# Optimization experiments

Measured on AMD Instinct MI355X. Metric: run time of the kernel, lower is better.

## Reference

```python
import jax, jax.numpy as jnp
import numpy as np
import math

DIM = 1024
H = 16
DH = DIM // H
B = 2
L = 1024


def setup_inputs() -> dict:
    key = jax.random.key(0)
    ks = jax.random.split(key, 8)
    s = 1.0 / math.sqrt(DIM)
    return {
        "Q": jax.random.normal(ks[0], (B, L, DIM), jnp.float32),
        "K": jax.random.normal(ks[1], (B, L, DIM), jnp.float32),
        "mask_Q": jax.random.bernoulli(ks[2], 0.1, (B, L)),
        "mask_K": jax.random.bernoulli(ks[3], 0.1, (B, L)),
        "Wq": jax.random.normal(ks[4], (DIM, DIM), jnp.float32) * s,
        "Wk": jax.random.normal(ks[5], (DIM, DIM), jnp.float32) * s,
        "Wv": jax.random.normal(ks[6], (DIM, DIM), jnp.float32) * s,
        "Wo": jax.random.normal(ks[7], (DIM, DIM), jnp.float32) * s,
    }


def reference(Q, K, mask_Q, mask_K, Wq, Wk, Wv, Wo):
    # V defaults to K. Masked positions of inputs are zeroed first.
    Qz = jnp.where(mask_Q[:, :, None], 0.0, Q)
    Kz = jnp.where(mask_K[:, :, None], 0.0, K)
    Vz = Kz  # V = K, masked with mask_K

    # Projections (nn.Linear, no bias): y = x @ W.T
    Qp = jnp.einsum('bld,ed->ble', Qz, Wq)
    Kp = jnp.einsum('bld,ed->ble', Kz, Wk)
    Vp = jnp.einsum('bld,ed->ble', Vz, Wv)

    # split heads: [B, L, H, DH] -> per-head attention
    qh = Qp.reshape(B, L, H, DH)
    kh = Kp.reshape(B, L, H, DH)
    vh = Vp.reshape(B, L, H, DH)

    # NOTE: original scales by sqrt(dim) (full dim), not sqrt(dim_split)
    scores = jnp.einsum('bqhd,bkhd->bhqk', qh, kh) / math.sqrt(DIM)

    # outer-product validity mask: valid iff both q and k positions unmasked
    valid = (~mask_Q)[:, None, :, None] & (~mask_K)[:, None, None, :]  # [B,1,Lq,Lk]
    A = jnp.where(valid, scores, -1e38)
    A = jax.nn.softmax(A, axis=-1)
    A = jnp.where(valid, A, 0.0)

    O = jnp.einsum('bhqk,bkhd->bqhd', A, vh).reshape(B, L, DIM)
    # residual uses the PROJECTED Q (Q was reassigned to fc_q(Q) in torch)
    O = Qp + O
    # masked_forward(fc_o, ...): fc_o applied, masked query rows forced to 0
    ff = jax.nn.relu(jnp.where(mask_Q[:, :, None], 0.0, jnp.einsum('bld,ed->ble', O, Wo)))
    O = O + ff
    return O
```

## Files before the change

kernel.cpp:

```cpp
#include <hip/hip_runtime.h>
#include <hip/hip_bf16.h>


#define DEV __device__ __forceinline__

typedef __attribute__((ext_vector_type(8))) short bf16x8;
typedef __attribute__((ext_vector_type(4))) float f32x4;
typedef __hip_bfloat16 bf16;

DEV void glds16(const bf16* g, bf16* s) {
  __builtin_amdgcn_global_load_lds(
      (const __attribute__((address_space(1))) void*)g,
      (__attribute__((address_space(3))) void*)s, 16, 0, 0);
}

DEV unsigned short f2bu(float x) {
  __hip_bfloat16 b = __float2bfloat16(x);
  unsigned short u;
  __builtin_memcpy(&u, &b, 2);
  return u;
}

DEV float bu2f(unsigned short u) {
  unsigned int v = (unsigned int)u << 16;
  float f;
  __builtin_memcpy(&f, &v, 4);
  return f;
}

__global__ void normalize_masks(const unsigned char* mq_raw, const unsigned char* mk_raw,
                                unsigned char* outq, unsigned char* outk,
                                unsigned long long* qm64, unsigned long long* km64) {
  __shared__ int cnt;
  int t = threadIdx.x;
  if (t == 0) cnt = 0;
  __syncthreads();
  int c = 0;
  for (int i = t; i < 2048; i += 256) c += (mq_raw[i] != 0);
  atomicAdd(&cnt, c);
  __syncthreads();
  bool isByte = cnt > 128;
  for (int i = t; i < 2048; i += 256) {
    unsigned char q, k;
    if (isByte) {
      q = (mq_raw[i] != 0); k = (mk_raw[i] != 0);
    } else {
      q = (((const int*)mq_raw)[i] != 0); k = (((const int*)mk_raw)[i] != 0);
    }
    outq[i] = q; outk[i] = k;
  }
  __syncthreads();
  if (t < 64) {
    const unsigned char* src = (t < 32) ? outk : outq;
    int idx = t & 31;
    unsigned long long m = 0;
    for (int j = 0; j < 64; ++j)
      m |= (unsigned long long)(src[idx * 64 + j] != 0) << j;
    if (t < 32) km64[idx] = m; else qm64[idx] = m;
  }
}

__global__ __launch_bounds__(256) void cast_all(
    const float* __restrict__ Q, const float* __restrict__ K,
    const unsigned char* __restrict__ mq, const unsigned char* __restrict__ mk,
    const float* __restrict__ W0, const float* __restrict__ W1,
    const float* __restrict__ W2, const float* __restrict__ W3,
    bf16* __restrict__ Qz, bf16* __restrict__ Kz,
    bf16* __restrict__ o0, bf16* __restrict__ o1,
    bf16* __restrict__ o2, bf16* __restrict__ o3) {
  const int z = blockIdx.z;
  if (z < 2) {
    const float* X = z ? K : Q;
    const unsigned char* m = z ? mk : mq;
    bf16* out = z ? Kz : Qz;
    int i = (blockIdx.x * 256 + threadIdx.x) * 8;
    float4 v0 = *(const float4*)&X[i];
    float4 v1 = *(const float4*)&X[i + 4];
    if (m[i >> 10]) {
      v0 = make_float4(0.f, 0.f, 0.f, 0.f);
      v1 = make_float4(0.f, 0.f, 0.f, 0.f);
    }
    *(ushort4*)&out[i] = make_ushort4(f2bu(v0.x), f2bu(v0.y), f2bu(v0.z), f2bu(v0.w));
    *(ushort4*)&out[i + 4] = make_ushort4(f2bu(v1.x), f2bu(v1.y), f2bu(v1.z), f2bu(v1.w));
  } else {
    const float* X; bf16* out;
    switch (z) {
      case 2: X = W0; out = o0; break;
      case 3: X = W1; out = o1; break;
      case 4: X = W2; out = o2; break;
      default: X = W3; out = o3; break;
    }
    int i = (blockIdx.x * 256 + threadIdx.x) * 4;
    float4 v = *(const float4*)&X[i];
    *(ushort4*)&out[i] = make_ushort4(f2bu(v.x), f2bu(v.y), f2bu(v.z), f2bu(v.w));
  }
}

template <int MI, int NI, typename EPI>
DEV void gemm_core(const bf16* __restrict__ A, const bf16* __restrict__ W,
                   int K, int brow, int bcol, EPI&& epi) {
  __shared__ bf16 As[2 * MI * 512];
  __shared__ bf16 Bs[2 * NI * 2048];
  const int t = threadIdx.x, l = t & 63, w = t >> 6;
  const int rs = l >> 2;
  const int kcol = (l & 3) * 8;

  f32x4 acc[MI][NI];
#pragma unroll
  for (int i = 0; i < MI; i++)
#pragma unroll
    for (int j = 0; j < NI; j++) acc[i][j] = (f32x4){0.f, 0.f, 0.f, 0.f};

  auto stage = [&](int k0, int b_) {
#pragma unroll
    for (int i = 0; i < MI; ++i)
      if ((i & 3) == w)
        glds16(A + (size_t)(brow + i * 16 + rs) * K + k0 + kcol,
               &As[b_ * MI * 512 + i * 512]);
#pragma unroll
    for (int c = 0; c < NI; ++c)
      glds16(W + (size_t)(bcol + (w * NI + c) * 16 + rs) * K + k0 + kcol,
             &Bs[b_ * NI * 2048 + (w * NI + c) * 512]);
  };

  const int aoff0 = (l & 15) * 32 + (l >> 4) * 8;
  const int boff0 = (w * NI * 16 + (l & 15)) * 32 + (l >> 4) * 8;

  stage(0, 0);
  int buf = 0;
  for (int k0 = 0; k0 < K; k0 += 32) {
    __syncthreads();
    if (k0 + 32 < K) stage(k0 + 32, buf ^ 1);
    bf16x8 a[MI], b[NI];
#pragma unroll
    for (int mi = 0; mi < MI; ++mi)
      a[mi] = *(const bf16x8*)&As[buf * MI * 512 + aoff0 + mi * 512];
#pragma unroll
    for (int ni = 0; ni < NI; ++ni)
      b[ni] = *(const bf16x8*)&Bs[buf * NI * 2048 + boff0 + ni * 512];
#pragma unroll
    for (int mi = 0; mi < MI; ++mi)
#pragma unroll
      for (int ni = 0; ni < NI; ++ni)
        acc[mi][ni] = __builtin_amdgcn_mfma_f32_16x16x32_bf16(a[mi], b[ni], acc[mi][ni], 0, 0, 0);
    buf ^= 1;
  }

#pragma unroll
  for (int mi = 0; mi < MI; ++mi)
#pragma unroll
    for (int ni = 0; ni < NI; ++ni)
#pragma unroll
      for (int r = 0; r < 4; ++r) {
        int row = brow + mi * 16 + (l >> 4) * 4 + r;
        int col = bcol + (w * NI + ni) * 16 + (l & 15);
        epi(row, col, acc[mi][ni][r]);
      }
}

__global__ __launch_bounds__(256) void proj_gemm(
    const bf16* __restrict__ Qz, const bf16* __restrict__ Kz,
    const bf16* __restrict__ Wq, const bf16* __restrict__ Wk, const bf16* __restrict__ Wv,
    bf16* __restrict__ Qpb, bf16* __restrict__ Kpb, bf16* __restrict__ Vpb) {
  const int z = blockIdx.z;
  const int brow = blockIdx.x * 64, bcol = blockIdx.y * 128;
  const bf16* A = (z == 0) ? Qz : Kz;
  const bf16* W = (z == 0) ? Wq : ((z == 1) ? Wk : Wv);
  bf16* dst = (z == 0) ? Qpb : ((z == 1) ? Kpb : Vpb);
  const float scale = (z == 0) ? 0.045084220f : 1.0f;
  gemm_core<4, 2>(A, W, 1024, brow, bcol, [&](int row, int col, float v) {
    dst[((size_t)row << 10) + col] = __float2bfloat16(v * scale);
  });
}

__global__ __launch_bounds__(256) void final_gemm(
    const bf16* __restrict__ Ob, const bf16* __restrict__ Wo,
    float* __restrict__ out, const unsigned char* __restrict__ mq) {
  const int brow = blockIdx.x * 64, bcol = blockIdx.y * 64;
  gemm_core<4, 1>(Ob, Wo, 1024, brow, bcol, [&](int row, int col, float v) {
    size_t idx = ((size_t)row << 10) + col;
    float ff = mq[row] ? 0.f : fmaxf(v, 0.f);
    out[idx] = out[idx] + ff;
  });
}

__global__ __launch_bounds__(256) void attn_fused(
    const bf16* __restrict__ Qpb, const bf16* __restrict__ Kpb, const bf16* __restrict__ Vpb,
    const unsigned long long* __restrict__ qm64, const unsigned long long* __restrict__ km64,
    float* __restrict__ Of, bf16* __restrict__ Ob) {
  __shared__ bf16 Klds[2][64 * 64];
  __shared__ bf16 Vt[64 * 72];

  const int t = threadIdx.x, l = t & 63, w = t >> 6;
  const int q = l & 15, g = l >> 4;
  const int f = blockIdx.x;
  const int bh = (f & 7) + 8 * ((f >> 3) & 3);
  const int qt = f >> 5;
  const int b = bh >> 4, h = bh & 15;
  const size_t bbase = (size_t)b * 1024;

  const int qg = qt * 64 + w * 16 + q;
  const bf16* qptr = Qpb + (bbase + qg) * 1024 + h * 64 + g * 8;
  const bf16x8 qb0 = *(const bf16x8*)qptr;
  const bf16x8 qb1 = *(const bf16x8*)(qptr + 32);

  float psum = 0.f;
  f32x4 oacc[4];
#pragma unroll
  for (int mf = 0; mf < 4; ++mf) oacc[mf] = (f32x4){0.f, 0.f, 0.f, 0.f};

  const int krow_s = l >> 3;
  const int kcol_s = ((l & 7) ^ krow_s) * 8;
  const int vk0 = 2 * (t & 31);
  const int vdc = t >> 5;

  union { uint4 v; unsigned short s[8]; } u0, u1;

  auto stageK = [&](int kt_, int b_) {
#pragma unroll
    for (int c = 0; c < 2; ++c) {
      int cw = w * 2 + c;
      glds16(Kpb + (bbase + kt_ * 64 + cw * 8 + krow_s) * 1024 + h * 64 + kcol_s,
             &Klds[b_][cw * 512]);
    }
  };
  auto loadV = [&](int kt_) {
    const bf16* g0 = Vpb + (bbase + kt_ * 64 + vk0) * 1024 + h * 64 + vdc * 8;
    u0.v = *(const uint4*)g0;
    u1.v = *(const uint4*)(g0 + 1024);
  };

  stageK(0, 0);
  loadV(0);
  int buf = 0;

  for (int kt = 0; kt < 16; ++kt) {
    const unsigned long long km = km64[b * 16 + kt];
    const unsigned long long mloc = km >> (4 * g);

    __syncthreads();

#pragma unroll
    for (int j = 0; j < 8; ++j) {
      unsigned int pk = (unsigned int)u0.s[j] | ((unsigned int)u1.s[j] << 16);
      *(unsigned int*)((char*)Vt + (vdc * 8 + j) * 144 + vk0 * 2) = pk;
    }

    f32x4 S[4];
#pragma unroll
    for (int mf = 0; mf < 4; ++mf) {
#pragma unroll
      for (int r = 0; r < 4; ++r)
        S[mf][r] = ((mloc >> (mf * 16 + r)) & 1ull) ? -1e30f : 0.f;
      const int row = mf * 16 + q;
      const int rowb = row * 128;
      const bf16x8 ka0 = *(const bf16x8*)((const char*)&Klds[buf][0] + rowb + ((g ^ (row & 7)) * 16));
      const bf16x8 ka1 = *(const bf16x8*)((const char*)&Klds[buf][0] + rowb + (((g + 4) ^ (row & 7)) * 16));
      S[mf] = __builtin_amdgcn_mfma_f32_16x16x32_bf16(ka0, qb0, S[mf], 0, 0, 0);
      S[mf] = __builtin_amdgcn_mfma_f32_16x16x32_bf16(ka1, qb1, S[mf], 0, 0, 0);
    }

    unsigned int lo[4], hi[4];
#pragma unroll
    for (int mf = 0; mf < 4; ++mf) {
      float p0 = exp2f(S[mf][0]), p1 = exp2f(S[mf][1]);
      float p2 = exp2f(S[mf][2]), p3 = exp2f(S[mf][3]);
      psum += (p0 + p1) + (p2 + p3);
      lo[mf] = (unsigned int)f2bu(p0) | ((unsigned int)f2bu(p1) << 16);
      hi[mf] = (unsigned int)f2bu(p2) | ((unsigned int)f2bu(p3) << 16);
    }

    __syncthreads();

    if (kt < 15) {
      stageK(kt + 1, buf ^ 1);
      loadV(kt + 1);
    }

    const int srcA = ((2 * g) & 3) * 16 + q;
    const int srcB = srcA + 16;
    const bool sel = (g >> 1) & 1;
#pragma unroll
    for (int ks = 0; ks < 2; ++ks) {
      unsigned int a0 = __shfl(lo[2 * ks], srcA), a1 = __shfl(hi[2 * ks], srcA);
      unsigned int a2 = __shfl(lo[2 * ks], srcB), a3 = __shfl(hi[2 * ks], srcB);
      unsigned int b0 = __shfl(lo[2 * ks + 1], srcA), b1 = __shfl(hi[2 * ks + 1], srcA);
      unsigned int b2 = __shfl(lo[2 * ks + 1], srcB), b3 = __shfl(hi[2 * ks + 1], srcB);
      uint4 pw;
      pw.x = sel ? b0 : a0; pw.y = sel ? b1 : a1;
      pw.z = sel ? b2 : a2; pw.w = sel ? b3 : a3;
      const bf16x8 pa = __builtin_bit_cast(bf16x8, pw);
#pragma unroll
      for (int mf = 0; mf < 4; ++mf) {
        const bf16x8 va = *(const bf16x8*)((const char*)Vt + (mf * 16 + q) * 144 + ks * 64 + g * 16);
        oacc[mf] = __builtin_amdgcn_mfma_f32_16x16x32_bf16(va, pa, oacc[mf], 0, 0, 0);
      }
    }
    buf ^= 1;
  }

  psum += __shfl_xor(psum, 16);
  psum += __shfl_xor(psum, 32);

  const unsigned long long qm = qm64[b * 16 + qt];
  const bool qvalid = !((qm >> (w * 16 + q)) & 1ull);
  const float inv = (qvalid && psum > 0.f) ? 1.f / psum : 0.f;
  const float RQ = 22.180709777918f;
#pragma unroll
  for (int mf = 0; mf < 4; ++mf) {
    size_t idx = (bbase + qg) * 1024 + h * 64 + mf * 16 + g * 4;
    ushort4 q4 = *(const ushort4*)&Qpb[idx];
    float4 val;
    val.x = bu2f(q4.x) * RQ + oacc[mf][0] * inv;
    val.y = bu2f(q4.y) * RQ + oacc[mf][1] * inv;
    val.z = bu2f(q4.z) * RQ + oacc[mf][2] * inv;
    val.w = bu2f(q4.w) * RQ + oacc[mf][3] * inv;
    *(float4*)&Of[idx] = val;
    *(ushort4*)&Ob[idx] = make_ushort4(f2bu(val.x), f2bu(val.y), f2bu(val.z), f2bu(val.w));
  }
}

extern "C" void kernel_launch(void* const* d_in, const int* in_sizes, int n_in,
                              void* d_out, int out_size, void* d_ws, size_t ws_size,
                              hipStream_t stream) {
  const float* Q = (const float*)d_in[0];
  const float* K = (const float*)d_in[1];
  const unsigned char* mQraw = (const unsigned char*)d_in[2];
  const unsigned char* mKraw = (const unsigned char*)d_in[3];
  const float* Wq = (const float*)d_in[4];
  const float* Wk = (const float*)d_in[5];
  const float* Wv = (const float*)d_in[6];
  const float* Wo = (const float*)d_in[7];
  float* out = (float*)d_out;

  char* ws = (char*)d_ws;
  const size_t MB = 1024 * 1024;
  bf16* Qz = (bf16*)(ws + 0);
  bf16* Kz = (bf16*)(ws + 4 * MB);
  bf16* Wqb = (bf16*)(ws + 8 * MB);
  bf16* Wkb = (bf16*)(ws + 10 * MB);
  bf16* Wvb = (bf16*)(ws + 12 * MB);
  bf16* Wob = (bf16*)(ws + 14 * MB);
  bf16* Qpb = (bf16*)(ws + 16 * MB);
  bf16* Kpb = (bf16*)(ws + 20 * MB);
  bf16* Vpb = (bf16*)(ws + 24 * MB);
  bf16* Ob  = (bf16*)(ws + 28 * MB);
  unsigned char* mqn = (unsigned char*)(ws + 32 * MB);
  unsigned char* mkn = mqn + 2048;
  unsigned long long* km64 = (unsigned long long*)(ws + 32 * MB + 4096);
  unsigned long long* qm64 = km64 + 32;

  normalize_masks<<<1, 256, 0, stream>>>(mQraw, mKraw, mqn, mkn, qm64, km64);

  dim3 gc(1024, 1, 6);
  cast_all<<<gc, 256, 0, stream>>>(Q, K, mqn, mkn, Wq, Wk, Wv, Wo,
                                   Qz, Kz, Wqb, Wkb, Wvb, Wob);

  dim3 gp(32, 8, 3);
  proj_gemm<<<gp, 256, 0, stream>>>(Qz, Kz, Wqb, Wkb, Wvb, Qpb, Kpb, Vpb);

  attn_fused<<<512, 256, 0, stream>>>(Qpb, Kpb, Vpb, qm64, km64, out, Ob);

  dim3 gf(32, 16);
  final_gemm<<<gf, 256, 0, stream>>>(Ob, Wob, out, mqn);
}
```

Before: 96.54 us.

## Fuse fp32-to-bf16 casting and input masking into projection and output GEMM loads

Removes the separate cast_all kernel. The projection and output GEMMs now read fp32 activations and weights directly, apply the masks and convert to bf16 in registers before writing to shared memory. This saves one launch and the bf16 intermediate write and read. In exchange, the GEMMs load twice the bytes per tile through registers instead of the async global-to-LDS path. Weights are reconverted by every block that reads them, so conversion work repeats across blocks.

```diff
diff --git a/kernel.cpp b/kernel.cpp
--- a/kernel.cpp
+++ b/kernel.cpp
@@ -26,6 +26,15 @@
   float f;
   __builtin_memcpy(&f, &v, 4);
   return f;
+}
+
+DEV bf16x8 cvt8(float4 a, float4 b) {
+  bf16x8 r;
+  r[0] = (short)f2bu(a.x); r[1] = (short)f2bu(a.y);
+  r[2] = (short)f2bu(a.z); r[3] = (short)f2bu(a.w);
+  r[4] = (short)f2bu(b.x); r[5] = (short)f2bu(b.y);
+  r[6] = (short)f2bu(b.z); r[7] = (short)f2bu(b.w);
+  return r;
 }
 
 __global__ void normalize_masks(const unsigned char* mq_raw, const unsigned char* mk_raw,
@@ -60,128 +69,150 @@
   }
 }
 
-__global__ __launch_bounds__(256) void cast_all(
-    const float* __restrict__ Q, const float* __restrict__ K,
-    const unsigned char* __restrict__ mq, const unsigned char* __restrict__ mk,
-    const float* __restrict__ W0, const float* __restrict__ W1,
-    const float* __restrict__ W2, const float* __restrict__ W3,
-    bf16* __restrict__ Qz, bf16* __restrict__ Kz,
-    bf16* __restrict__ o0, bf16* __restrict__ o1,
-    bf16* __restrict__ o2, bf16* __restrict__ o3) {
+__global__ __launch_bounds__(256) void proj_gemm(
+    const float* __restrict__ Qf, const float* __restrict__ Kf,
+    const float* __restrict__ Wq, const float* __restrict__ Wk, const float* __restrict__ Wv,
+    const unsigned char* __restrict__ mqn, const unsigned char* __restrict__ mkn,
+    bf16* __restrict__ Qpb, bf16* __restrict__ Kpb, bf16* __restrict__ Vpb) {
+  __shared__ bf16 As[2][4 * 512];
+  __shared__ bf16 Bs[2][8 * 512];
   const int z = blockIdx.z;
-  if (z < 2) {
-    const float* X = z ? K : Q;
-    const unsigned char* m = z ? mk : mq;
-    bf16* out = z ? Kz : Qz;
-    int i = (blockIdx.x * 256 + threadIdx.x) * 8;
-    float4 v0 = *(const float4*)&X[i];
-    float4 v1 = *(const float4*)&X[i + 4];
-    if (m[i >> 10]) {
-      v0 = make_float4(0.f, 0.f, 0.f, 0.f);
-      v1 = make_float4(0.f, 0.f, 0.f, 0.f);
-    }
-    *(ushort4*)&out[i] = make_ushort4(f2bu(v0.x), f2bu(v0.y), f2bu(v0.z), f2bu(v0.w));
-    *(ushort4*)&out[i + 4] = make_ushort4(f2bu(v1.x), f2bu(v1.y), f2bu(v1.z), f2bu(v1.w));
-  } else {
-    const float* X; bf16* out;
-    switch (z) {
-      case 2: X = W0; out = o0; break;
-      case 3: X = W1; out = o1; break;
-      case 4: X = W2; out = o2; break;
-      default: X = W3; out = o3; break;
-    }
-    int i = (blockIdx.x * 256 + threadIdx.x) * 4;
-    float4 v = *(const float4*)&X[i];
-    *(ushort4*)&out[i] = make_ushort4(f2bu(v.x), f2bu(v.y), f2bu(v.z), f2bu(v.w));
-  }
-}
-
-template <int MI, int NI, typename EPI>
-DEV void gemm_core(const bf16* __restrict__ A, const bf16* __restrict__ W,
-                   int K, int brow, int bcol, EPI&& epi) {
-  __shared__ bf16 As[2 * MI * 512];
-  __shared__ bf16 Bs[2 * NI * 2048];
+  const int brow = blockIdx.x * 64, bcol = blockIdx.y * 128;
+  const float* A = (z == 0) ? Qf : Kf;
+  const float* W = (z == 0) ? Wq : ((z == 1) ? Wk : Wv);
+  const unsigned char* am = (z == 0) ? mqn : mkn;
+  bf16* dst = (z == 0) ? Qpb : ((z == 1) ? Kpb : Vpb);
+  const float scale = (z == 0) ? 0.045084220f : 1.0f;
+
   const int t = threadIdx.x, l = t & 63, w = t >> 6;
   const int rs = l >> 2;
   const int kcol = (l & 3) * 8;
 
-  f32x4 acc[MI][NI];
-#pragma unroll
-  for (int i = 0; i < MI; i++)
-#pragma unroll
-    for (int j = 0; j < NI; j++) acc[i][j] = (f32x4){0.f, 0.f, 0.f, 0.f};
-
-  auto stage = [&](int k0, int b_) {
-#pragma unroll
-    for (int i = 0; i < MI; ++i)
-      if ((i & 3) == w)
-        glds16(A + (size_t)(brow + i * 16 + rs) * K + k0 + kcol,
-               &As[b_ * MI * 512 + i * 512]);
-#pragma unroll
-    for (int c = 0; c < NI; ++c)
-      glds16(W + (size_t)(bcol + (w * NI + c) * 16 + rs) * K + k0 + kcol,
-             &Bs[b_ * NI * 2048 + (w * NI + c) * 512]);
+  const int arow = brow + w * 16 + rs;
+  const float* Aptr = A + (size_t)arow * 1024 + kcol;
+  const bool amask = (am[arow] != 0);
+  const float* Bptr0 = W + (size_t)(bcol + (w * 2 + 0) * 16 + rs) * 1024 + kcol;
+  const float* Bptr1 = W + (size_t)(bcol + (w * 2 + 1) * 16 + rs) * 1024 + kcol;
+
+  f32x4 acc[4][2];
+#pragma unroll
+  for (int i = 0; i < 4; i++)
+#pragma unroll
+    for (int j = 0; j < 2; j++) acc[i][j] = (f32x4){0.f, 0.f, 0.f, 0.f};
+
+  float4 va0, va1, vb00, vb01, vb10, vb11;
+  auto ld = [&](int k0) {
+    va0 = *(const float4*)(Aptr + k0);
+    va1 = *(const float4*)(Aptr + k0 + 4);
+    vb00 = *(const float4*)(Bptr0 + k0);
+    vb01 = *(const float4*)(Bptr0 + k0 + 4);
+    vb10 = *(const float4*)(Bptr1 + k0);
+    vb11 = *(const float4*)(Bptr1 + k0 + 4);
+  };
+  const float4 z4 = make_float4(0.f, 0.f, 0.f, 0.f);
+  auto cvtwrite = [&](int b_) {
+    *(bf16x8*)&As[b_][w * 512 + rs * 32 + kcol] = cvt8(amask ? z4 : va0, amask ? z4 : va1);
+    *(bf16x8*)&Bs[b_][(w * 2 + 0) * 512 + rs * 32 + kcol] = cvt8(vb00, vb01);
+    *(bf16x8*)&Bs[b_][(w * 2 + 1) * 512 + rs * 32 + kcol] = cvt8(vb10, vb11);
   };
 
   const int aoff0 = (l & 15) * 32 + (l >> 4) * 8;
-  const int boff0 = (w * NI * 16 + (l & 15)) * 32 + (l >> 4) * 8;
-
-  stage(0, 0);
+  const int boff0 = (w * 32 + (l & 15)) * 32 + (l >> 4) * 8;
+
+  ld(0);
+  cvtwrite(0);
   int buf = 0;
-  for (int k0 = 0; k0 < K; k0 += 32) {
+  for (int k0 = 0; k0 < 1024; k0 += 32) {
     __syncthreads();
-    if (k0 + 32 < K) stage(k0 + 32, buf ^ 1);
-    bf16x8 a[MI], b[NI];
-#pragma unroll
-    for (int mi = 0; mi < MI; ++mi)
-      a[mi] = *(const bf16x8*)&As[buf * MI * 512 + aoff0 + mi * 512];
-#pragma unroll
-    for (int ni = 0; ni < NI; ++ni)
-      b[ni] = *(const bf16x8*)&Bs[buf * NI * 2048 + boff0 + ni * 512];
-#pragma unroll
-    for (int mi = 0; mi < MI; ++mi)
-#pragma unroll
-      for (int ni = 0; ni < NI; ++ni)
+    if (k0 + 32 < 1024) ld(k0 + 32);
+    bf16x8 a[4], b[2];
+#pragma unroll
+    for (int mi = 0; mi < 4; ++mi) a[mi] = *(const bf16x8*)&As[buf][aoff0 + mi * 512];
+#pragma unroll
+    for (int ni = 0; ni < 2; ++ni) b[ni] = *(const bf16x8*)&Bs[buf][boff0 + ni * 512];
+#pragma unroll
+    for (int mi = 0; mi < 4; ++mi)
+#pragma unroll
+      for (int ni = 0; ni < 2; ++ni)
         acc[mi][ni] = __builtin_amdgcn_mfma_f32_16x16x32_bf16(a[mi], b[ni], acc[mi][ni], 0, 0, 0);
+    if (k0 + 32 < 1024) cvtwrite(buf ^ 1);
     buf ^= 1;
   }
 
 #pragma unroll
-  for (int mi = 0; mi < MI; ++mi)
-#pragma unroll
-    for (int ni = 0; ni < NI; ++ni)
+  for (int mi = 0; mi < 4; ++mi)
+#pragma unroll
+    for (int ni = 0; ni < 2; ++ni)
 #pragma unroll
       for (int r = 0; r < 4; ++r) {
         int row = brow + mi * 16 + (l >> 4) * 4 + r;
-        int col = bcol + (w * NI + ni) * 16 + (l & 15);
-        epi(row, col, acc[mi][ni][r]);
+        int col = bcol + (w * 2 + ni) * 16 + (l & 15);
+        dst[((size_t)row << 10) + col] = __float2bfloat16(acc[mi][ni][r] * scale);
       }
 }
 
-__global__ __launch_bounds__(256) void proj_gemm(
-    const bf16* __restrict__ Qz, const bf16* __restrict__ Kz,
-    const bf16* __restrict__ Wq, const bf16* __restrict__ Wk, const bf16* __restrict__ Wv,
-    bf16* __restrict__ Qpb, bf16* __restrict__ Kpb, bf16* __restrict__ Vpb) {
-  const int z = blockIdx.z;
-  const int brow = blockIdx.x * 64, bcol = blockIdx.y * 128;
-  const bf16* A = (z == 0) ? Qz : Kz;
-  const bf16* W = (z == 0) ? Wq : ((z == 1) ? Wk : Wv);
-  bf16* dst = (z == 0) ? Qpb : ((z == 1) ? Kpb : Vpb);
-  const float scale = (z == 0) ? 0.045084220f : 1.0f;
-  gemm_core<4, 2>(A, W, 1024, brow, bcol, [&](int row, int col, float v) {
-    dst[((size_t)row << 10) + col] = __float2bfloat16(v * scale);
-  });
-}
-
 __global__ __launch_bounds__(256) void final_gemm(
-    const bf16* __restrict__ Ob, const bf16* __restrict__ Wo,
+    const bf16* __restrict__ Ob, const float* __restrict__ Wo,
     float* __restrict__ out, const unsigned char* __restrict__ mq) {
+  __shared__ bf16 As[2][4 * 512];
+  __shared__ bf16 Bs[2][4 * 512];
   const int brow = blockIdx.x * 64, bcol = blockIdx.y * 64;
-  gemm_core<4, 1>(Ob, Wo, 1024, brow, bcol, [&](int row, int col, float v) {
-    size_t idx = ((size_t)row << 10) + col;
-    float ff = mq[row] ? 0.f : fmaxf(v, 0.f);
-    out[idx] = out[idx] + ff;
-  });
+  const int t = threadIdx.x, l = t & 63, w = t >> 6;
+  const int rs = l >> 2;
+  const int kcol = (l & 3) * 8;
+
+  const float* Bptr = Wo + (size_t)(bcol + w * 16 + rs) * 1024 + kcol;
+
+  f32x4 acc[4];
+#pragma unroll
+  for (int i = 0; i < 4; i++) acc[i] = (f32x4){0.f, 0.f, 0.f, 0.f};
+
+  float4 vb0, vb1;
+  auto stageA = [&](int k0, int b_) {
+    glds16(Ob + (size_t)(brow + w * 16 + rs) * 1024 + k0 + kcol, &As[b_][w * 512]);
+  };
+  auto ldB = [&](int k0) {
+    vb0 = *(const float4*)(Bptr + k0);
+    vb1 = *(const float4*)(Bptr + k0 + 4);
+  };
+  auto cvtwriteB = [&](int b_) {
+    *(bf16x8*)&Bs[b_][w * 512 + rs * 32 + kcol] = cvt8(vb0, vb1);
+  };
+
+  const int aoff0 = (l & 15) * 32 + (l >> 4) * 8;
+  const int boff0 = (w * 16 + (l & 15)) * 32 + (l >> 4) * 8;
+
+  stageA(0, 0);
+  ldB(0);
+  cvtwriteB(0);
+  int buf = 0;
+  for (int k0 = 0; k0 < 1024; k0 += 32) {
+    __syncthreads();
+    if (k0 + 32 < 1024) {
+      stageA(k0 + 32, buf ^ 1);
+      ldB(k0 + 32);
+    }
+    bf16x8 a[4], b;
+#pragma unroll
+    for (int mi = 0; mi < 4; ++mi) a[mi] = *(const bf16x8*)&As[buf][aoff0 + mi * 512];
+    b = *(const bf16x8*)&Bs[buf][boff0];
+#pragma unroll
+    for (int mi = 0; mi < 4; ++mi)
+      acc[mi] = __builtin_amdgcn_mfma_f32_16x16x32_bf16(a[mi], b, acc[mi], 0, 0, 0);
+    if (k0 + 32 < 1024) cvtwriteB(buf ^ 1);
+    buf ^= 1;
+  }
+
+#pragma unroll
+  for (int mi = 0; mi < 4; ++mi)
+#pragma unroll
+    for (int r = 0; r < 4; ++r) {
+      int row = brow + mi * 16 + (l >> 4) * 4 + r;
+      int col = bcol + w * 16 + (l & 15);
+      size_t idx = ((size_t)row << 10) + col;
+      float ff = mq[row] ? 0.f : fmaxf(acc[mi][r], 0.f);
+      out[idx] = out[idx] + ff;
+    }
 }
 
 __global__ __launch_bounds__(256) void attn_fused(
@@ -335,32 +366,22 @@
 
   char* ws = (char*)d_ws;
   const size_t MB = 1024 * 1024;
-  bf16* Qz = (bf16*)(ws + 0);
-  bf16* Kz = (bf16*)(ws + 4 * MB);
-  bf16* Wqb = (bf16*)(ws + 8 * MB);
-  bf16* Wkb = (bf16*)(ws + 10 * MB);
-  bf16* Wvb = (bf16*)(ws + 12 * MB);
-  bf16* Wob = (bf16*)(ws + 14 * MB);
-  bf16* Qpb = (bf16*)(ws + 16 * MB);
-  bf16* Kpb = (bf16*)(ws + 20 * MB);
-  bf16* Vpb = (bf16*)(ws + 24 * MB);
-  bf16* Ob  = (bf16*)(ws + 28 * MB);
-  unsigned char* mqn = (unsigned char*)(ws + 32 * MB);
+  bf16* Qpb = (bf16*)(ws + 0);
+  bf16* Kpb = (bf16*)(ws + 4 * MB);
+  bf16* Vpb = (bf16*)(ws + 8 * MB);
+  bf16* Ob  = (bf16*)(ws + 12 * MB);
+  unsigned char* mqn = (unsigned char*)(ws + 16 * MB);
   unsigned char* mkn = mqn + 2048;
-  unsigned long long* km64 = (unsigned long long*)(ws + 32 * MB + 4096);
+  unsigned long long* km64 = (unsigned long long*)(ws + 16 * MB + 8192);
   unsigned long long* qm64 = km64 + 32;
 
   normalize_masks<<<1, 256, 0, stream>>>(mQraw, mKraw, mqn, mkn, qm64, km64);
 
-  dim3 gc(1024, 1, 6);
-  cast_all<<<gc, 256, 0, stream>>>(Q, K, mqn, mkn, Wq, Wk, Wv, Wo,
-                                   Qz, Kz, Wqb, Wkb, Wvb, Wob);
-
   dim3 gp(32, 8, 3);
-  proj_gemm<<<gp, 256, 0, stream>>>(Qz, Kz, Wqb, Wkb, Wvb, Qpb, Kpb, Vpb);
+  proj_gemm<<<gp, 256, 0, stream>>>(Q, K, Wq, Wk, Wv, mqn, mkn, Qpb, Kpb, Vpb);
 
   attn_fused<<<512, 256, 0, stream>>>(Qpb, Kpb, Vpb, qm64, km64, out, Ob);
 
   dim3 gf(32, 16);
-  final_gemm<<<gf, 256, 0, stream>>>(Ob, Wob, out, mqn);
-}
+  final_gemm<<<gf, 256, 0, stream>>>(Ob, Wo, out, mqn);
+}
```

Result: no change. 97.80 us (+1.3%).

## Write V projection transposed per head and read K/V directly from global in attention

Applied to the files above, without the earlier changes.

The V projection epilogue now writes a per-head transposed layout (VpT), so the attention kernel can load V fragments straight from global memory without the LDS transpose. K is likewise read directly from global, which removes the shared-memory staging and both block barriers per tile. Launch bounds now request two blocks per SM. The weight cast path also moves to 8 elements per thread with half the blocks. The trade is losing LDS reuse and the software prefetch in favour of relying on caches, with the transposed V store scattered across strided rows.

```diff
diff --git a/kernel.cpp b/kernel.cpp
--- a/kernel.cpp
+++ b/kernel.cpp
@@ -83,6 +83,7 @@
     *(ushort4*)&out[i] = make_ushort4(f2bu(v0.x), f2bu(v0.y), f2bu(v0.z), f2bu(v0.w));
     *(ushort4*)&out[i + 4] = make_ushort4(f2bu(v1.x), f2bu(v1.y), f2bu(v1.z), f2bu(v1.w));
   } else {
+    if (blockIdx.x >= 512) return;
     const float* X; bf16* out;
     switch (z) {
       case 2: X = W0; out = o0; break;
@@ -90,9 +91,11 @@
       case 4: X = W2; out = o2; break;
       default: X = W3; out = o3; break;
     }
-    int i = (blockIdx.x * 256 + threadIdx.x) * 4;
-    float4 v = *(const float4*)&X[i];
-    *(ushort4*)&out[i] = make_ushort4(f2bu(v.x), f2bu(v.y), f2bu(v.z), f2bu(v.w));
+    int i = (blockIdx.x * 256 + threadIdx.x) * 8;
+    float4 v0 = *(const float4*)&X[i];
+    float4 v1 = *(const float4*)&X[i + 4];
+    *(ushort4*)&out[i] = make_ushort4(f2bu(v0.x), f2bu(v0.y), f2bu(v0.z), f2bu(v0.w));
+    *(ushort4*)&out[i + 4] = make_ushort4(f2bu(v1.x), f2bu(v1.y), f2bu(v1.z), f2bu(v1.w));
   }
 }
 
@@ -149,27 +152,37 @@
 #pragma unroll
   for (int mi = 0; mi < MI; ++mi)
 #pragma unroll
-    for (int ni = 0; ni < NI; ++ni)
-#pragma unroll
-      for (int r = 0; r < 4; ++r) {
-        int row = brow + mi * 16 + (l >> 4) * 4 + r;
-        int col = bcol + (w * NI + ni) * 16 + (l & 15);
-        epi(row, col, acc[mi][ni][r]);
-      }
+    for (int ni = 0; ni < NI; ++ni) {
+      int row0 = brow + mi * 16 + (l >> 4) * 4;
+      int col = bcol + (w * NI + ni) * 16 + (l & 15);
+      epi(row0, col, acc[mi][ni]);
+    }
 }
 
 __global__ __launch_bounds__(256) void proj_gemm(
     const bf16* __restrict__ Qz, const bf16* __restrict__ Kz,
     const bf16* __restrict__ Wq, const bf16* __restrict__ Wk, const bf16* __restrict__ Wv,
-    bf16* __restrict__ Qpb, bf16* __restrict__ Kpb, bf16* __restrict__ Vpb) {
+    bf16* __restrict__ Qpb, bf16* __restrict__ Kpb, bf16* __restrict__ VpT) {
   const int z = blockIdx.z;
   const int brow = blockIdx.x * 64, bcol = blockIdx.y * 128;
   const bf16* A = (z == 0) ? Qz : Kz;
   const bf16* W = (z == 0) ? Wq : ((z == 1) ? Wk : Wv);
-  bf16* dst = (z == 0) ? Qpb : ((z == 1) ? Kpb : Vpb);
-  const float scale = (z == 0) ? 0.045084220f : 1.0f;
-  gemm_core<4, 2>(A, W, 1024, brow, bcol, [&](int row, int col, float v) {
-    dst[((size_t)row << 10) + col] = __float2bfloat16(v * scale);
+  gemm_core<4, 2>(A, W, 1024, brow, bcol, [&](int row0, int col, f32x4 v) {
+    if (z == 2) {
+      int b_ = row0 >> 10, tok = row0 & 1023;
+      int hh = col >> 6, dd = col & 63;
+      size_t base = ((size_t)((b_ * 16 + hh) * 64 + dd) << 10) + tok;
+      *(ushort4*)&VpT[base] = make_ushort4(f2bu(v[0]), f2bu(v[1]), f2bu(v[2]), f2bu(v[3]));
+    } else if (z == 0) {
+      const float scale = 0.045084220f;
+#pragma unroll
+      for (int r = 0; r < 4; ++r)
+        Qpb[((size_t)(row0 + r) << 10) + col] = __float2bfloat16(v[r] * scale);
+    } else {
+#pragma unroll
+      for (int r = 0; r < 4; ++r)
+        Kpb[((size_t)(row0 + r) << 10) + col] = __float2bfloat16(v[r]);
+    }
   });
 }
 
@@ -177,20 +190,20 @@
     const bf16* __restrict__ Ob, const bf16* __restrict__ Wo,
     float* __restrict__ out, const unsigned char* __restrict__ mq) {
   const int brow = blockIdx.x * 64, bcol = blockIdx.y * 64;
-  gemm_core<4, 1>(Ob, Wo, 1024, brow, bcol, [&](int row, int col, float v) {
-    size_t idx = ((size_t)row << 10) + col;
-    float ff = mq[row] ? 0.f : fmaxf(v, 0.f);
-    out[idx] = out[idx] + ff;
+  gemm_core<4, 1>(Ob, Wo, 1024, brow, bcol, [&](int row0, int col, f32x4 v) {
+#pragma unroll
+    for (int r = 0; r < 4; ++r) {
+      size_t idx = ((size_t)(row0 + r) << 10) + col;
+      float ff = mq[row0 + r] ? 0.f : fmaxf(v[r], 0.f);
+      out[idx] = out[idx] + ff;
+    }
   });
 }
 
-__global__ __launch_bounds__(256) void attn_fused(
-    const bf16* __restrict__ Qpb, const bf16* __restrict__ Kpb, const bf16* __restrict__ Vpb,
+__global__ __launch_bounds__(256, 2) void attn_fused(
+    const bf16* __restrict__ Qpb, const bf16* __restrict__ Kpb, const bf16* __restrict__ VpT,
     const unsigned long long* __restrict__ qm64, const unsigned long long* __restrict__ km64,
     float* __restrict__ Of, bf16* __restrict__ Ob) {
-  __shared__ bf16 Klds[2][64 * 64];
-  __shared__ bf16 Vt[64 * 72];
-
   const int t = threadIdx.x, l = t & 63, w = t >> 6;
   const int q = l & 15, g = l >> 4;
   const int f = blockIdx.x;
@@ -204,47 +217,22 @@
   const bf16x8 qb0 = *(const bf16x8*)qptr;
   const bf16x8 qb1 = *(const bf16x8*)(qptr + 32);
 
+  const bf16* Kbase = Kpb + bbase * 1024 + h * 64;
+  const bf16* Vbase = VpT + ((size_t)(b * 16 + h) << 16);
+
   float psum = 0.f;
   f32x4 oacc[4];
 #pragma unroll
   for (int mf = 0; mf < 4; ++mf) oacc[mf] = (f32x4){0.f, 0.f, 0.f, 0.f};
 
-  const int krow_s = l >> 3;
-  const int kcol_s = ((l & 7) ^ krow_s) * 8;
-  const int vk0 = 2 * (t & 31);
-  const int vdc = t >> 5;
-
-  union { uint4 v; unsigned short s[8]; } u0, u1;
-
-  auto stageK = [&](int kt_, int b_) {
-#pragma unroll
-    for (int c = 0; c < 2; ++c) {
-      int cw = w * 2 + c;
-      glds16(Kpb + (bbase + kt_ * 64 + cw * 8 + krow_s) * 1024 + h * 64 + kcol_s,
-             &Klds[b_][cw * 512]);
-    }
-  };
-  auto loadV = [&](int kt_) {
-    const bf16* g0 = Vpb + (bbase + kt_ * 64 + vk0) * 1024 + h * 64 + vdc * 8;
-    u0.v = *(const uint4*)g0;
-    u1.v = *(const uint4*)(g0 + 1024);
-  };
-
-  stageK(0, 0);
-  loadV(0);
-  int buf = 0;
-
+  const int srcA = ((2 * g) & 3) * 16 + q;
+  const int srcB = srcA + 16;
+  const bool sel = (g >> 1) & 1;
+
+#pragma unroll 2
   for (int kt = 0; kt < 16; ++kt) {
-    const unsigned long long km = km64[b * 16 + kt];
-    const unsigned long long mloc = km >> (4 * g);
-
-    __syncthreads();
-
-#pragma unroll
-    for (int j = 0; j < 8; ++j) {
-      unsigned int pk = (unsigned int)u0.s[j] | ((unsigned int)u1.s[j] << 16);
-      *(unsigned int*)((char*)Vt + (vdc * 8 + j) * 144 + vk0 * 2) = pk;
-    }
+    const int kbase = kt * 64;
+    const unsigned long long mloc = km64[b * 16 + kt] >> (4 * g);
 
     f32x4 S[4];
 #pragma unroll
@@ -252,10 +240,9 @@
 #pragma unroll
       for (int r = 0; r < 4; ++r)
         S[mf][r] = ((mloc >> (mf * 16 + r)) & 1ull) ? -1e30f : 0.f;
-      const int row = mf * 16 + q;
-      const int rowb = row * 128;
-      const bf16x8 ka0 = *(const bf16x8*)((const char*)&Klds[buf][0] + rowb + ((g ^ (row & 7)) * 16));
-      const bf16x8 ka1 = *(const bf16x8*)((const char*)&Klds[buf][0] + rowb + (((g + 4) ^ (row & 7)) * 16));
+      const bf16* kr = Kbase + (size_t)(kbase + mf * 16 + q) * 1024 + g * 8;
+      const bf16x8 ka0 = *(const bf16x8*)kr;
+      const bf16x8 ka1 = *(const bf16x8*)(kr + 32);
       S[mf] = __builtin_amdgcn_mfma_f32_16x16x32_bf16(ka0, qb0, S[mf], 0, 0, 0);
       S[mf] = __builtin_amdgcn_mfma_f32_16x16x32_bf16(ka1, qb1, S[mf], 0, 0, 0);
     }
@@ -270,16 +257,6 @@
       hi[mf] = (unsigned int)f2bu(p2) | ((unsigned int)f2bu(p3) << 16);
     }
 
-    __syncthreads();
-
-    if (kt < 15) {
-      stageK(kt + 1, buf ^ 1);
-      loadV(kt + 1);
-    }
-
-    const int srcA = ((2 * g) & 3) * 16 + q;
-    const int srcB = srcA + 16;
-    const bool sel = (g >> 1) & 1;
 #pragma unroll
     for (int ks = 0; ks < 2; ++ks) {
       unsigned int a0 = __shfl(lo[2 * ks], srcA), a1 = __shfl(hi[2 * ks], srcA);
@@ -292,11 +269,11 @@
       const bf16x8 pa = __builtin_bit_cast(bf16x8, pw);
 #pragma unroll
       for (int mf = 0; mf < 4; ++mf) {
-        const bf16x8 va = *(const bf16x8*)((const char*)Vt + (mf * 16 + q) * 144 + ks * 64 + g * 16);
+        const bf16x8 va = *(const bf16x8*)(Vbase + (size_t)(mf * 16 + q) * 1024 +
+                                           kbase + ks * 32 + g * 8);
         oacc[mf] = __builtin_amdgcn_mfma_f32_16x16x32_bf16(va, pa, oacc[mf], 0, 0, 0);
       }
     }
-    buf ^= 1;
   }
 
   psum += __shfl_xor(psum, 16);
@@ -335,19 +312,19 @@
 
   char* ws = (char*)d_ws;
   const size_t MB = 1024 * 1024;
-  bf16* Qz = (bf16*)(ws + 0);
-  bf16* Kz = (bf16*)(ws + 4 * MB);
+  bf16* Qz  = (bf16*)(ws + 0);
+  bf16* Kz  = (bf16*)(ws + 4 * MB);
   bf16* Wqb = (bf16*)(ws + 8 * MB);
   bf16* Wkb = (bf16*)(ws + 10 * MB);
   bf16* Wvb = (bf16*)(ws + 12 * MB);
   bf16* Wob = (bf16*)(ws + 14 * MB);
   bf16* Qpb = (bf16*)(ws + 16 * MB);
   bf16* Kpb = (bf16*)(ws + 20 * MB);
-  bf16* Vpb = (bf16*)(ws + 24 * MB);
+  bf16* VpT = (bf16*)(ws + 24 * MB);
   bf16* Ob  = (bf16*)(ws + 28 * MB);
   unsigned char* mqn = (unsigned char*)(ws + 32 * MB);
   unsigned char* mkn = mqn + 2048;
-  unsigned long long* km64 = (unsigned long long*)(ws + 32 * MB + 4096);
+  unsigned long long* km64 = (unsigned long long*)(ws + 32 * MB + 8192);
   unsigned long long* qm64 = km64 + 32;
 
   normalize_masks<<<1, 256, 0, stream>>>(mQraw, mKraw, mqn, mkn, qm64, km64);
@@ -357,9 +334,9 @@
                                    Qz, Kz, Wqb, Wkb, Wvb, Wob);
 
   dim3 gp(32, 8, 3);
-  proj_gemm<<<gp, 256, 0, stream>>>(Qz, Kz, Wqb, Wkb, Wvb, Qpb, Kpb, Vpb);
-
-  attn_fused<<<512, 256, 0, stream>>>(Qpb, Kpb, Vpb, qm64, km64, out, Ob);
+  proj_gemm<<<gp, 256, 0, stream>>>(Qz, Kz, Wqb, Wkb, Wvb, Qpb, Kpb, VpT);
+
+  attn_fused<<<512, 256, 0, stream>>>(Qpb, Kpb, VpT, qm64, km64, out, Ob);
 
   dim3 gf(32, 16);
   final_gemm<<<gf, 256, 0, stream>>>(Ob, Wob, out, mqn);
```

Measured after the change: 134.4 us. 1.39x slower.
